# Kernel tuning notes

Hardware: AMD Instinct MI355X
Metric: run time of the kernel (lower is better)

Reference implementation:

```python
import jax, jax.numpy as jnp
import numpy as np
import math

B, H, M, L, D = 4, 8, 512, 2048, 64   # batch, heads, block len, span, head dim
RAMP = 64                              # adapt_span_len (soft-mask ramp size)


def setup_inputs() -> dict:
    key = jax.random.key(0)
    ks = jax.random.split(key, 5)
    BH = B * H
    KL = M + L
    return {
        "query": jax.random.normal(ks[0], (BH, M, D), jnp.float32),
        "key_": jax.random.normal(ks[1], (BH, KL, D), jnp.float32),
        "value": jax.random.normal(ks[2], (BH, KL, D), jnp.float32),
        "key_pe": jax.random.normal(ks[3], (1, D, L), jnp.float32) * 0.02,
        "current_val": jax.random.uniform(ks[4], (H, 1, 1), jnp.float32, minval=0.3, maxval=0.9),
    }


def reference(query, key_, value, key_pe, current_val):
    BH, Mq, Dh = query.shape
    KL = key_.shape[1]
    Lw = KL - Mq  # attention span
    nb = BH // current_val.shape[0]  # batch size (heads folded into leading dim)

    # full scores then unskew: band[b, i, j] = scores[b, i, i + j]
    scores = jnp.einsum('bmd,bnd->bmn', query, key_)              # (BH, M, M+L)
    rows = jnp.arange(Mq)[:, None]                                # (M, 1)
    band_idx = rows + jnp.arange(Lw)[None, :]                     # (M, L)
    attn = scores[:, rows, band_idx]                              # (BH, M, L)

    # relative position bias, scale, softmax
    attn = attn + jnp.einsum('bmd,dl->bml', query, key_pe[0])
    attn = attn / math.sqrt(Dh)
    attn = jax.nn.softmax(attn, axis=-1)

    # adaptive span soft mask (per head) + renormalization
    template = jnp.arange(1 - Lw, 1, dtype=attn.dtype)            # (L,) = linspace(1-L, 0, L)
    mask = jnp.clip((template + current_val * Lw) / RAMP + 1.0, 0.0, 1.0)  # (H, 1, L)
    attn4 = attn.reshape(nb, -1, Mq, Lw) * mask[None]             # (B, H, M, L)
    attn4 = attn4 / (attn4.sum(-1, keepdims=True) + 1e-8)
    attn = attn4.reshape(BH, Mq, Lw)

    # skew back to (BH, M, M+L) and contract with values
    skewed = jnp.zeros((BH, Mq, KL), attn.dtype).at[:, rows, band_idx].set(attn)
    out = jnp.einsum('bmn,bnd->bmd', skewed, value)               # (BH, M, D)
    return out
```

## Files before the change

kernel.cpp:

```cpp
#include <hip/hip_runtime.h>
#include <math.h>

typedef _Float16 half_t;
typedef _Float16 half8 __attribute__((ext_vector_type(8)));
typedef _Float16 half4 __attribute__((ext_vector_type(4)));
typedef _Float16 half2v __attribute__((ext_vector_type(2)));
typedef float f32x4 __attribute__((ext_vector_type(4)));
typedef float f32x16 __attribute__((ext_vector_type(16)));
typedef unsigned int uint4v __attribute__((ext_vector_type(4)));

#define MFMA_S(a, b, c) __builtin_amdgcn_mfma_f32_32x32x16_f16((a), (b), (c), 0, 0, 0)

static constexpr int kM  = 512;
static constexpr int kD  = 64;
static constexpr int kKL = 2560;
static constexpr int kL  = 2048;
static constexpr int WS_QS  = 0;
static constexpr int WS_KB  = 1048576;
static constexpr int WS_VC  = WS_KB + 5242880;
static constexpr int WS_PET = WS_VC + 5242880;
static constexpr size_t WS_ZP_B = 23330816;
static constexpr size_t WS_PO_B = WS_ZP_B + 262144;

__global__ __launch_bounds__(256) void prep_kernel(const float* __restrict__ q,
    const float* __restrict__ k, const float* __restrict__ v,
    const float* __restrict__ pe, half_t* __restrict__ ws) {
  __shared__ float ls[64 * 72];
  const int b = blockIdx.x, t = threadIdx.x;
  if (b < 3072) {
    const int i = b * 256 + t;
    const float QS = 0.125f * 1.4426950408889634f;
    const float* src; half_t* dst; float sc;
    if (i < 131072) { src = q + (size_t)i * 8; dst = ws + WS_QS + (size_t)i * 8; sc = QS; }
    else { const int j = i - 131072; src = k + (size_t)j * 8; dst = ws + WS_KB + (size_t)j * 8; sc = 1.0f; }
    const float4 a = ((const float4*)src)[0];
    const float4 bb = ((const float4*)src)[1];
    half_t tt[8];
    tt[0] = (half_t)(a.x * sc);  tt[1] = (half_t)(a.y * sc);
    tt[2] = (half_t)(a.z * sc);  tt[3] = (half_t)(a.w * sc);
    tt[4] = (half_t)(bb.x * sc); tt[5] = (half_t)(bb.y * sc);
    tt[6] = (half_t)(bb.z * sc); tt[7] = (half_t)(bb.w * sc);
    *(int4*)dst = *(int4*)tt;
    return;
  }
  const bool isV = (b < 4352);
  int bh = 0, kt = 0, b3 = 0;
  const float* src; int sstride;
  if (isV) {
    const int b2 = b - 3072;
    bh = b2 / 40; kt = b2 % 40;
    src = v + (size_t)(bh * 2560 + kt * 64) * 64; sstride = 64;
  } else {
    b3 = b - 4352;
    src = pe + (size_t)b3 * 64; sstride = 2048;
  }
  const int rr = t >> 4, cq = (t & 15) * 4;
#pragma unroll
  for (int p = 0; p < 4; ++p) {
    const float4 x = *(const float4*)(src + (size_t)(p * 16 + rr) * sstride + cq);
    *(float4*)(ls + (p * 16 + rr) * 72 + cq) = x;
  }
  __syncthreads();
  const int oc = t >> 2, ch = t & 3;
  half_t tmp[16];
#pragma unroll
  for (int i2 = 0; i2 < 16; ++i2) tmp[i2] = (half_t)ls[(ch * 16 + i2) * 72 + oc];
  half_t* o;
  if (isV) {
    o = ws + WS_VC + (size_t)bh * 163840 + ((kt << 1) + (ch >> 1)) * 2048 + oc * 32 + ((ch & 1) << 4);
  } else {
    o = ws + WS_PET + ((size_t)b3 * 64 + oc) * 64 + ch * 16;
  }
  ((int4*)o)[0] = ((int4*)tmp)[0];
  ((int4*)o)[1] = ((int4*)tmp)[1];
}

__global__ __launch_bounds__(256, 2) void attn_kernel(
    const half_t* __restrict__ ws, const float* __restrict__ cvp,
    float* __restrict__ po, float* __restrict__ zp) {

  __shared__ __align__(16) char smem[36864];
  half_t* lsh = (half_t*)smem;

  const int tid  = threadIdx.x;
  const int lane = tid & 63;
  const int w    = tid >> 6;
  const int c32  = lane & 31;
  const int h    = lane >> 5;

  const int id = blockIdx.x;
  const int bh = ((id & 7) << 2) | (id >> 7);
  const int mid = (id >> 3) & 15;
  const int mb = mid & 3, sp = mid >> 2;
  const int m0 = mb << 7;
  const int g0 = sp * 17;

  const float cvl = cvp[bh & 7] * 2048.0f - 2047.0f;
  const float cvO = cvl * 0.015625f + 1.0f;

  const half_t* kb  = ws + WS_KB + (size_t)bh * (kKL * kD);
  const half_t* vcb = ws + WS_VC + (size_t)bh * (kKL * kD);
  const half_t* pet = ws + WS_PET;

  const half_t* qrow = ws + WS_QS + (size_t)(bh * kM + m0 + 32 * w + c32) * kD;
  half8 bq[4];
#pragma unroll
  for (int t = 0; t < 4; ++t) bq[t] = *(const half8*)(qrow + t * 16 + h * 8);

  half_t* stf = lsh + 9728 + w * 2176 + c32 * 68;

  int4 stgK, stgV;
  auto issueKV = [&](int gg) {
    const int r = tid >> 3, seg = tid & 7;
    const int krow = m0 + (gg << 5) + r;
    stgK = *(const int4*)(kb + (size_t)krow * kD + seg * 8);
    const int vch = (m0 >> 5) + gg;
    stgV = *(const int4*)(vcb + (size_t)vch * 2048 + tid * 8);
  };
  auto commitKV = [&](int gg) {
    const int sK = (gg & 1) * 2304;
    const int sV = 4608 + (gg & 1) * 2560;
    const int r = tid >> 3, seg = tid & 7;
    *(int4*)(lsh + sK + r * 72 + seg * 8) = stgK;
    const int d = tid >> 2, ks = (tid & 3) * 8;
    *(int4*)(lsh + sV + d * 40 + ks) = stgV;
  };

  auto peWindow = [&](int wb) -> f32x16 {
    int l = wb + c32; l = l < 0 ? 0 : (l > kL - 1 ? kL - 1 : l);
    const half_t* pp = pet + (size_t)l * kD;
    f32x16 a = {};
#pragma unroll
    for (int t = 0; t < 4; ++t) {
      const half8 p = *(const half8*)(pp + t * 16 + h * 8);
      a = MFMA_S(p, bq[t], a);
    }
    return a;
  };
  auto stripWrite = [&](int wb, const f32x16& a) {
    const int allone  = (wb >= 0) && (wb + 31 <= kL - 1) && (wb + cvl >= 0.0f);
    const int allzero = (wb > kL - 1) || (wb + 31 < 0) || ((float)(wb + 31) + cvl <= -64.0f);
#pragma unroll
    for (int reg = 0; reg < 16; ++reg) {
      const int lr = (reg & 3) + 8 * (reg >> 2) + 4 * h;
      const int l  = wb + lr;
      float bl;
      if (allzero) bl = -HUGE_VALF;
      else if (allone) bl = a[reg];
      else {
        const float mk = fminf(fmaxf((float)l * 0.015625f + cvO, 0.0f), 1.0f);
        const float lg = __builtin_amdgcn_logf(mk);
        bl = ((unsigned)l < (unsigned)kL) ? a[reg] + lg : -HUGE_VALF;
      }
      stf[(l + c32) & 63] = (half_t)bl;
    }
  };

  issueKV(g0);
  const int B0 = (g0 << 5) - 32 * w;
  stripWrite(B0 - 32, peWindow(B0 - 32));
  stripWrite(B0,      peWindow(B0));
  commitKV(g0);
  __syncthreads();

  float zmc = 0.0f;
  f32x16 o0 = {}, o1 = {};

  for (int t = 0; t < 17; ++t) {
    const int g = g0 + t;
    const bool more = (t < 16);
    if (more) issueKV(g + 1);

    const int sK = (g & 1) * 2304;
    const int sV = 4608 + (g & 1) * 2560;
    const int B = (g << 5) - 32 * w;

    half8 ak[4];
#pragma unroll
    for (int kt = 0; kt < 4; ++kt)
      ak[kt] = *(const half8*)(lsh + sK + c32 * 72 + kt * 16 + h * 8);

    half4 emq[4];
#pragma unroll
    for (int q = 0; q < 4; ++q)
      emq[q] = *(const half4*)(stf + ((B + 8 * q + 4 * h) & 63));

    half8 av[2][2];
#pragma unroll
    for (int dh = 0; dh < 2; ++dh)
#pragma unroll
      for (int kt = 0; kt < 2; ++kt)
        av[dh][kt] = *(const half8*)(lsh + sV + (32 * dh + c32) * 40 + kt * 16 + h * 8);

    f32x16 s = {};
#pragma unroll
    for (int kt = 0; kt < 4; ++kt) s = MFMA_S(ak[kt], bq[kt], s);

    float pm[16];
#pragma unroll
    for (int reg = 0; reg < 16; ++reg) {
      pm[reg] = __builtin_amdgcn_exp2f(s[reg] + (float)emq[reg >> 2][reg & 3]);
      zmc += pm[reg];
    }
    unsigned Wp[8];
#pragma unroll
    for (int q = 0; q < 8; ++q) {
      const half2v hp = { (half_t)pm[2 * q], (half_t)pm[2 * q + 1] };
      Wp[q] = __builtin_bit_cast(unsigned, hp);
    }
    const auto r0 = __builtin_amdgcn_permlane32_swap(Wp[0], Wp[2], false, false);
    const auto r1 = __builtin_amdgcn_permlane32_swap(Wp[1], Wp[3], false, false);
    const auto r2 = __builtin_amdgcn_permlane32_swap(Wp[4], Wp[6], false, false);
    const auto r3 = __builtin_amdgcn_permlane32_swap(Wp[5], Wp[7], false, false);
    const uint4v u0 = { (unsigned)r0[0], (unsigned)r1[0], (unsigned)r0[1], (unsigned)r1[1] };
    const uint4v u1 = { (unsigned)r2[0], (unsigned)r3[0], (unsigned)r2[1], (unsigned)r3[1] };
    const half8 pb0 = __builtin_bit_cast(half8, u0);
    const half8 pb1 = __builtin_bit_cast(half8, u1);

    o0 = MFMA_S(av[0][0], pb0, o0);
    o0 = MFMA_S(av[0][1], pb1, o0);
    o1 = MFMA_S(av[1][0], pb0, o1);
    o1 = MFMA_S(av[1][1], pb1, o1);

    if (more) {
      stripWrite(B + 32, peWindow(B + 32));
      commitKV(g + 1);
    }
    __syncthreads();
  }

  float* Ow = (float*)smem + (size_t)w * 2176;
#pragma unroll
  for (int q = 0; q < 4; ++q) {
    *(f32x4*)(Ow + c32 * 68 + 0  + 8 * q + 4 * h) =
        f32x4{o0[q * 4], o0[q * 4 + 1], o0[q * 4 + 2], o0[q * 4 + 3]};
    *(f32x4*)(Ow + c32 * 68 + 32 + 8 * q + 4 * h) =
        f32x4{o1[q * 4], o1[q * 4 + 1], o1[q * 4 + 2], o1[q * 4 + 3]};
  }
  zmc += __shfl_xor(zmc, 32);
  const int rowbase = bh * kM + m0 + 32 * w;
  if (lane < 32) zp[(size_t)sp * 16384 + rowbase + c32] = zmc;
  float* pob = po + ((size_t)sp * 16384 + rowbase) * 64;
#pragma unroll
  for (int u = 0; u < 8; ++u) {
    const int row = u * 4 + (lane >> 4);
    const int d4 = (lane & 15) << 2;
    *(f32x4*)(pob + (size_t)row * 64 + d4) = *(const f32x4*)(Ow + row * 68 + d4);
  }
}

__global__ __launch_bounds__(256) void norm_kernel(const float* __restrict__ zp,
    const float* __restrict__ po, float* __restrict__ out) {
  const int i = blockIdx.x * 256 + threadIdx.x;
  const int row = i >> 4, d4 = (i & 15) << 2;
  const float z = zp[row] + zp[16384 + row] + zp[32768 + row] + zp[49152 + row];
  const float inv = 1.0f / (z + 1e-20f);
  f32x4 a = *(const f32x4*)(po + (size_t)row * 64 + d4);
  const f32x4 b = *(const f32x4*)(po + 1048576u + (size_t)row * 64 + d4);
  const f32x4 c = *(const f32x4*)(po + 2097152u + (size_t)row * 64 + d4);
  const f32x4 d = *(const f32x4*)(po + 3145728u + (size_t)row * 64 + d4);
  a = a + b + c + d;
  *(f32x4*)(out + (size_t)row * 64 + d4) = a * inv;
}

extern "C" void kernel_launch(void* const* d_in, const int* in_sizes, int n_in,
                              void* d_out, int out_size, void* d_ws, size_t ws_size,
                              hipStream_t stream) {
  (void)in_sizes; (void)n_in; (void)out_size; (void)ws_size;
  const float* q  = (const float*)d_in[0];
  const float* k  = (const float*)d_in[1];
  const float* v  = (const float*)d_in[2];
  const float* pe = (const float*)d_in[3];
  const float* cv = (const float*)d_in[4];
  half_t* ws = (half_t*)d_ws;
  float* out = (float*)d_out;
  float* zp = (float*)((char*)d_ws + WS_ZP_B);
  float* po = (float*)((char*)d_ws + WS_PO_B);

  prep_kernel<<<4384, 256, 0, stream>>>(q, k, v, pe, ws);
  attn_kernel<<<512, 256, 0, stream>>>(ws, cv, po, zp);
  norm_kernel<<<1024, 256, 0, stream>>>(zp, po, out);
}
```

Before: 134.5 us.

## Process two K/V tiles per barrier with a 4-deep LDS ring and early PE loads

The main loop now handles two 32-row K/V tiles per iteration. It uses a four-slot shared-memory ring, so one __syncthreads covers two steps instead of one, and the global loads for the next two tiles are issued ahead. The positional-embedding rows are loaded before the compute steps so their latency overlaps the MFMAs. The bias is fed into the score MFMA accumulator instead of being added afterwards, and LDS row strides change (66/34). The cost is more LDS (51200 B), which may limit blocks per CU, plus more live registers for the doubled staging.

Result: slower. 162.0 us (+20.5%).

```diff
diff --git a/kernel.cpp b/kernel.cpp
--- a/kernel.cpp
+++ b/kernel.cpp
@@ -79,7 +79,7 @@
     const half_t* __restrict__ ws, const float* __restrict__ cvp,
     float* __restrict__ po, float* __restrict__ zp) {
 
-  __shared__ __align__(16) char smem[36864];
+  __shared__ __align__(16) char smem[51200];
   half_t* lsh = (half_t*)smem;
 
   const int tid  = threadIdx.x;
@@ -107,34 +107,35 @@
 #pragma unroll
   for (int t = 0; t < 4; ++t) bq[t] = *(const half8*)(qrow + t * 16 + h * 8);
 
-  half_t* stf = lsh + 9728 + w * 2176 + c32 * 68;
-
-  int4 stgK, stgV;
-  auto issueKV = [&](int gg) {
+  half_t* stf = lsh + 17152 + w * 2112 + c32 * 66;
+
+  int4 sK0, sV0, sK1, sV1;
+  auto issueKV = [&](int gg, int4& oK, int4& oV) {
     const int r = tid >> 3, seg = tid & 7;
     const int krow = m0 + (gg << 5) + r;
-    stgK = *(const int4*)(kb + (size_t)krow * kD + seg * 8);
+    oK = *(const int4*)(kb + (size_t)krow * kD + seg * 8);
     const int vch = (m0 >> 5) + gg;
-    stgV = *(const int4*)(vcb + (size_t)vch * 2048 + tid * 8);
-  };
-  auto commitKV = [&](int gg) {
-    const int sK = (gg & 1) * 2304;
-    const int sV = 4608 + (gg & 1) * 2560;
+    oV = *(const int4*)(vcb + (size_t)vch * 2048 + tid * 8);
+  };
+  auto commitKV = [&](int gg, const int4& iK, const int4& iV) {
+    half_t* kbf = lsh + (gg & 3) * 2112;
+    half_t* vbf = lsh + 8448 + (gg & 3) * 2176;
     const int r = tid >> 3, seg = tid & 7;
-    *(int4*)(lsh + sK + r * 72 + seg * 8) = stgK;
+    *(int4*)(kbf + r * 66 + seg * 8) = iK;
     const int d = tid >> 2, ks = (tid & 3) * 8;
-    *(int4*)(lsh + sV + d * 40 + ks) = stgV;
-  };
-
-  auto peWindow = [&](int wb) -> f32x16 {
+    *(int4*)(vbf + d * 34 + ks) = iV;
+  };
+
+  auto petLoad = [&](int wb, half8* p) {
     int l = wb + c32; l = l < 0 ? 0 : (l > kL - 1 ? kL - 1 : l);
     const half_t* pp = pet + (size_t)l * kD;
+#pragma unroll
+    for (int t = 0; t < 4; ++t) p[t] = *(const half8*)(pp + t * 16 + h * 8);
+  };
+  auto peMFMA = [&](const half8* p) -> f32x16 {
     f32x16 a = {};
 #pragma unroll
-    for (int t = 0; t < 4; ++t) {
-      const half8 p = *(const half8*)(pp + t * 16 + h * 8);
-      a = MFMA_S(p, bq[t], a);
-    }
+    for (int t = 0; t < 4; ++t) a = MFMA_S(p[t], bq[t], a);
     return a;
   };
   auto stripWrite = [&](int wb, const f32x16& a) {
@@ -156,50 +157,41 @@
     }
   };
 
-  issueKV(g0);
-  const int B0 = (g0 << 5) - 32 * w;
-  stripWrite(B0 - 32, peWindow(B0 - 32));
-  stripWrite(B0,      peWindow(B0));
-  commitKV(g0);
-  __syncthreads();
-
   float zmc = 0.0f;
   f32x16 o0 = {}, o1 = {};
 
-  for (int t = 0; t < 17; ++t) {
-    const int g = g0 + t;
-    const bool more = (t < 16);
-    if (more) issueKV(g + 1);
-
-    const int sK = (g & 1) * 2304;
-    const int sV = 4608 + (g & 1) * 2560;
+  auto doStep = [&](int g, const half8* ppre, bool produce) {
+    half_t* kbf = lsh + (g & 3) * 2112;
+    half_t* vbf = lsh + 8448 + (g & 3) * 2176;
     const int B = (g << 5) - 32 * w;
-
-    half8 ak[4];
-#pragma unroll
-    for (int kt = 0; kt < 4; ++kt)
-      ak[kt] = *(const half8*)(lsh + sK + c32 * 72 + kt * 16 + h * 8);
 
     half4 emq[4];
 #pragma unroll
     for (int q = 0; q < 4; ++q)
       emq[q] = *(const half4*)(stf + ((B + 8 * q + 4 * h) & 63));
 
+    half8 ak[4];
+#pragma unroll
+    for (int kt = 0; kt < 4; ++kt)
+      ak[kt] = *(const half8*)(kbf + c32 * 66 + kt * 16 + h * 8);
+
     half8 av[2][2];
 #pragma unroll
     for (int dh = 0; dh < 2; ++dh)
 #pragma unroll
       for (int kt = 0; kt < 2; ++kt)
-        av[dh][kt] = *(const half8*)(lsh + sV + (32 * dh + c32) * 40 + kt * 16 + h * 8);
-
-    f32x16 s = {};
+        av[dh][kt] = *(const half8*)(vbf + (32 * dh + c32) * 34 + kt * 16 + h * 8);
+
+    f32x16 s;
+#pragma unroll
+    for (int reg = 0; reg < 16; ++reg) s[reg] = (float)emq[reg >> 2][reg & 3];
 #pragma unroll
     for (int kt = 0; kt < 4; ++kt) s = MFMA_S(ak[kt], bq[kt], s);
 
     float pm[16];
 #pragma unroll
     for (int reg = 0; reg < 16; ++reg) {
-      pm[reg] = __builtin_amdgcn_exp2f(s[reg] + (float)emq[reg >> 2][reg & 3]);
+      pm[reg] = __builtin_amdgcn_exp2f(s[reg]);
       zmc += pm[reg];
     }
     unsigned Wp[8];
@@ -222,13 +214,38 @@
     o1 = MFMA_S(av[1][0], pb0, o1);
     o1 = MFMA_S(av[1][1], pb1, o1);
 
-    if (more) {
-      stripWrite(B + 32, peWindow(B + 32));
-      commitKV(g + 1);
-    }
+    if (produce) stripWrite(B + 32, peMFMA(ppre));
+  };
+
+  issueKV(g0,     sK0, sV0);
+  issueKV(g0 + 1, sK1, sV1);
+  const int B0 = (g0 << 5) - 32 * w;
+  {
+    half8 pq[4];
+    petLoad(B0 - 32, pq); stripWrite(B0 - 32, peMFMA(pq));
+    petLoad(B0,      pq); stripWrite(B0,      peMFMA(pq));
+  }
+  commitKV(g0,     sK0, sV0);
+  commitKV(g0 + 1, sK1, sV1);
+  __syncthreads();
+
+  half8 pp1[4], pp2[4];
+  for (int p = 0; p < 8; ++p) {
+    const int g = g0 + 2 * p;
+    const int B = (g << 5) - 32 * w;
+    issueKV(g + 2, sK0, sV0);
+    issueKV(p < 7 ? g + 3 : g + 2, sK1, sV1);
+    petLoad(B + 32, pp1);
+    petLoad(B + 64, pp2);
+    doStep(g,     pp1, true);
+    doStep(g + 1, pp2, true);
+    commitKV(g + 2, sK0, sV0);
+    commitKV(g + 3, sK1, sV1);
     __syncthreads();
   }
-
+  doStep(g0 + 16, pp1, false);
+
+  __syncthreads();
   float* Ow = (float*)smem + (size_t)w * 2176;
 #pragma unroll
   for (int q = 0; q < 4; ++q) {
@@ -240,6 +257,7 @@
   zmc += __shfl_xor(zmc, 32);
   const int rowbase = bh * kM + m0 + 32 * w;
   if (lane < 32) zp[(size_t)sp * 16384 + rowbase + c32] = zmc;
+  __syncthreads();
   float* pob = po + ((size_t)sp * 16384 + rowbase) * 64;
 #pragma unroll
   for (int u = 0; u < 8; ++u) {
```
